# Performance work log

Measured on AMD Instinct MI355X. Metric: run time of the kernel, lower is better.

## Reference

```python
import jax, jax.numpy as jnp
import numpy as np

E = 1024
BUCKET = 16
TAU = 0.75
ITERS = 8
SCALE = E ** -0.5
EPS = 1e-6


def _gumbel(rng, shape):
    u = jax.random.uniform(rng, shape, jnp.float32, 0.0, 1.0)
    return -jnp.log(-jnp.log(u + EPS) + EPS)


def _log_sinkhorn(log_alpha, n_iter):
    def body(i, la):
        la = la - jax.scipy.special.logsumexp(la, axis=-1, keepdims=True)
        la = la - jax.scipy.special.logsumexp(la, axis=-2, keepdims=True)
        return la
    return jnp.exp(jax.lax.fori_loop(0, n_iter, body, log_alpha))


def setup_inputs() -> dict:
    rng = jax.random.key(0)
    ks = jax.random.split(rng, 9)
    T, B, S = 4096, 8, 4096
    w = 0.02
    return {
        "query": jax.random.normal(ks[0], (T, B, E), jnp.float32),
        "key": jax.random.normal(ks[1], (S, B, E), jnp.float32),
        "value": jax.random.normal(ks[2], (S, B, E), jnp.float32),
        "wq": jax.random.normal(ks[3], (E, E), jnp.float32) * w,
        "bq": jnp.zeros((E,), jnp.float32),
        "wk": jax.random.normal(ks[4], (E, E), jnp.float32) * w,
        "bk": jnp.zeros((E,), jnp.float32),
        "wo": jax.random.normal(ks[5], (E, E), jnp.float32) * w,
        "bo": jnp.zeros((E,), jnp.float32),
    }


def reference(query, key, value, wq, bq, wk, bk, wo, bo):
    T, B, _ = query.shape
    S = key.shape[0]
    # projections (Linear: x @ W.T + b), move to (B, T, E)
    q = jnp.einsum('tbe,fe->btf', query, wq) + bq
    k = jnp.einsum('sbe,fe->bsf', key, wk) + bk
    v = jnp.transpose(value, (1, 0, 2))  # (B, S, E)
    nb, nkb = T // BUCKET, S // BUCKET
    # bucket aggregation: mean-pool q/k, flatten v buckets
    qb = q.reshape(B, nb, BUCKET, E).mean(axis=2)          # (B, nb, E)
    kb = k.reshape(B, nkb, BUCKET, E).mean(axis=2)         # (B, nkb, E)
    vb = v.reshape(B, nkb, BUCKET * E)                     # (B, nkb, BUCKET*E)
    # dot energy
    logits = jnp.einsum('bqe,bke->bqk', qb, kb) * SCALE    # (B, nb, nkb)
    log_alpha = logits
    # gumbel-sinkhorn (noise=True)
    g = _gumbel(jax.random.key(42), logits.shape)
    attn_weights = _log_sinkhorn((logits.astype(jnp.float32) + g) / TAU, ITERS)
    # attend on flattened buckets, then un-aggregate
    attn = jnp.einsum('bqk,bkd->bqd', attn_weights, vb)    # (B, nb, BUCKET*E)
    attn = attn.reshape(B, nb * BUCKET, E)
    attn = jnp.transpose(attn, (1, 0, 2))                  # (T, B, E)
    out = jnp.einsum('tbe,fe->tbf', attn, wo) + bo
    return out, attn_weights, log_alpha
```

## Files before the change

kernel.cpp:

```cpp
#include <hip/hip_runtime.h>


typedef float    f32x4 __attribute__((ext_vector_type(4)));
typedef _Float16 h4    __attribute__((ext_vector_type(4)));
typedef _Float16 h8    __attribute__((ext_vector_type(8)));

#define OUT_ELEMS 33554432
#define AW_ELEMS  524288

__device__ __forceinline__ void gload16(const void* g, void* l) {
  __builtin_amdgcn_global_load_lds((__attribute__((address_space(1))) void*)g,
                                   (__attribute__((address_space(3))) void*)l,
                                   16, 0, 0);
}

__global__ __launch_bounds__(256) void cb_k(const float* __restrict__ wq,
                                            const float* __restrict__ wk,
                                            const float* __restrict__ wo,
                                            _Float16* __restrict__ wdst,
                                            const float* __restrict__ q,
                                            const float* __restrict__ k,
                                            _Float16* __restrict__ qbar,
                                            _Float16* __restrict__ kbar) {
  __shared__ __attribute__((aligned(16))) float ldsbuf[8192];
  int bid = blockIdx.x;
  int tid = threadIdx.x;
  if (bid < 3072) {
    int which = bid >> 10;
    const float* src = which == 0 ? wq : (which == 1 ? wk : wo);
    size_t idx = (size_t)(bid & 1023) * 256 + tid;
    f32x4 v = ((const f32x4*)src)[idx];
    ((h4*)(wdst + (size_t)which * 1048576))[idx] = __builtin_convertvector(v, h4);
  } else {
    int g = bid - 3072;
    int srcid = g >> 12, ii = (g >> 4) & 255, bb = (g >> 1) & 7, eh = g & 1;
    const float* s2 = srcid ? k : q;
    _Float16* d2 = srcid ? kbar : qbar;
    const int grp = tid >> 7;
    const int wh  = (tid >> 6) & 1;
    const int col = tid & 127;
    #pragma unroll
    for (int jj = 0; jj < 8; ++jj) {
      int j = jj * 2 + grp;
      gload16(s2 + (size_t)((ii * 16 + j) * 8 + bb) * 1024 + eh * 512 + col * 4,
              &ldsbuf[j * 512 + wh * 256]);
    }
    __syncthreads();
    if (tid < 128) {
      f32x4 a = {0.f, 0.f, 0.f, 0.f};
      #pragma unroll
      for (int j = 0; j < 16; ++j)
        a += *(const f32x4*)&ldsbuf[j * 512 + tid * 4];
      a *= 0.0625f;
      ((h4*)(d2 + (size_t)(bb * 256 + ii) * 1024 + eh * 512))[tid] =
          __builtin_convertvector(a, h4);
    }
  }
}

__device__ __forceinline__ unsigned rotl32(unsigned x, int r) {
  return (x << r) | (x >> (32 - r));
}
__global__ __launch_bounds__(256) void gumbel_k(const float* __restrict__ logits,
                                                float* __restrict__ ebuf) {
  unsigned i = blockIdx.x * 256 + threadIdx.x;
  const unsigned k0 = 0u, k1 = 42u, k2 = 0u ^ 42u ^ 0x1BD11BDAu;
  unsigned x0 = 0u + k0, x1 = i + k1;
#define R4(a,b,c,d) \
  x0 += x1; x1 = rotl32(x1, a); x1 ^= x0; \
  x0 += x1; x1 = rotl32(x1, b); x1 ^= x0; \
  x0 += x1; x1 = rotl32(x1, c); x1 ^= x0; \
  x0 += x1; x1 = rotl32(x1, d); x1 ^= x0;
  R4(13,15,26,6)  x0 += k1; x1 += k2 + 1u;
  R4(17,29,16,24) x0 += k2; x1 += k0 + 2u;
  R4(13,15,26,6)  x0 += k0; x1 += k1 + 3u;
  R4(17,29,16,24) x0 += k1; x1 += k2 + 4u;
  R4(13,15,26,6)  x0 += k2; x1 += k0 + 5u;
#undef R4
  unsigned bits = x0 ^ x1;
  float u = __builtin_bit_cast(float, (bits >> 9) | 0x3f800000u) - 1.0f;
  float g = -logf(-logf(u + 1e-6f) + 1e-6f);
  ebuf[i] = __expf((logits[i] + g) / 0.75f);
}

__global__ __launch_bounds__(1024) void sinkvt_k(const float* __restrict__ ein,
                                                 float* __restrict__ attnw,
                                                 _Float16* __restrict__ wsh,
                                                 const float* __restrict__ v,
                                                 _Float16* __restrict__ vt) {
  __shared__ __attribute__((aligned(16))) char smem[36864];
  const int t = threadIdx.x;
  if (blockIdx.x < 8) {
    const int b = blockIdx.x;
    const int r = t >> 2, p = t & 3;
    const int k = t & 255, g = t >> 8;
    const float* Eb = ein + (size_t)b * 65536;
    const f32x4* Eb4 = (const f32x4*)Eb;
    float* ra = (float*)smem;
    float* cb = ra + 256;
    float (*part)[256] = (float (*)[256])(cb + 256);
    if (t < 256) cb[t] = 1.0f;
    __syncthreads();
    const f32x4* cb4 = (const f32x4*)cb;

    for (int it = 0; it < 8; ++it) {
      float s = 0.f;
      #pragma unroll
      for (int i = 0; i < 16; ++i) {
        f32x4 e = Eb4[r * 64 + p * 16 + i];
        f32x4 c = cb4[p * 16 + i];
        f32x4 m = e * c;
        s += (m[0] + m[1]) + (m[2] + m[3]);
      }
      s += __shfl_xor(s, 1, 64);
      s += __shfl_xor(s, 2, 64);
      if (p == 0) ra[r] = 1.0f / s;
      __syncthreads();
      float s2 = 0.f;
      #pragma unroll 8
      for (int q2 = 0; q2 < 64; ++q2) {
        int row = g * 64 + q2;
        s2 += Eb[row * 256 + k] * ra[row];
      }
      part[g][k] = s2;
      __syncthreads();
      if (t < 256) {
        cb[t] = 1.0f / (part[0][t] + part[1][t] + part[2][t] + part[3][t]);
      }
      __syncthreads();
    }

    const float arow = ra[r];
    f32x4* aw = (f32x4*)(attnw + (size_t)b * 65536 + r * 256 + p * 64);
    h4* wh = (h4*)(wsh + (size_t)b * 65536 + r * 256 + p * 64);
    #pragma unroll
    for (int i = 0; i < 16; ++i) {
      f32x4 e = Eb4[r * 64 + p * 16 + i];
      f32x4 c = cb4[p * 16 + i];
      f32x4 w = e * c * arow;
      aw[i] = w;
      h4 hv;
      hv[0] = (_Float16)w[0]; hv[1] = (_Float16)w[1];
      hv[2] = (_Float16)w[2]; hv[3] = (_Float16)w[3];
      wh[i] = hv;
    }
  } else {
    const int s = t >> 8, t2 = t & 255;
    int bid = (blockIdx.x - 8) * 4 + s;
    _Float16 (*tile)[72] = (_Float16 (*)[72])(smem + s * 9216);
    int kb = bid & 3, eb = (bid >> 2) & 15, j = (bid >> 6) & 15;
    int b = ((bid >> 10) + (bid & 7)) & 7;
    int k0 = kb * 64, e0 = eb * 64;
    int r = t2 >> 2, qq = t2 & 3;
    const float* src = v + ((size_t)((k0 + r) * 16 + j) * 8 + b) * 1024 + e0;
    #pragma unroll
    for (int ii = 0; ii < 4; ++ii) {
      f32x4 x = ((const f32x4*)src)[qq + ii * 4];
      *(h4*)&tile[r][(qq + ii * 4) * 4] = __builtin_convertvector(x, h4);
    }
    __syncthreads();
    _Float16* dstp = vt + (((size_t)(b * 16 + j) * 1024 + e0 + r) * 256 + k0 + qq * 16);
    h8 o0, o1;
    #pragma unroll
    for (int kk = 0; kk < 8; ++kk) o0[kk] = tile[qq * 16 + kk][r];
    #pragma unroll
    for (int kk = 0; kk < 8; ++kk) o1[kk] = tile[qq * 16 + 8 + kk][r];
    *(h8*)dstp = o0;
    *(h8*)(dstp + 8) = o1;
  }
}

template <int MODE>
__global__ __launch_bounds__(256) void gemm128(const _Float16* __restrict__ A,
                                               const _Float16* __restrict__ B,
                                               const float* __restrict__ bias,
                                               const float* __restrict__ bias2,
                                               void* __restrict__ out0,
                                               int K, int lda, int ldb) {
  const int tid = threadIdx.x, lane = tid & 63, w = tid >> 6;
  int bx = blockIdx.x, by = blockIdx.y, bz = blockIdx.z;
  if constexpr (MODE == 0) {
    int wid = ((bx & 7) << 4) + (bx >> 3);
    by = wid & 7; bx = wid >> 3;
  }
  if constexpr (MODE == 2) {
    int wid = ((bx & 7) << 8) + (bx >> 3);
    bz = wid >> 4; by = (wid >> 1) & 7; bx = wid & 1;
  }
  const int m0 = bx * 128, n0 = by * 128;
  const _Float16* Ab = A;
  const _Float16* Bb = B;
  const float* bs = bias;
  if constexpr (MODE == 0) {
    Ab += (size_t)bz * 2097152;
    Bb += (size_t)bz * 1048576;
    if (bz) bs = bias2;
  }
  if constexpr (MODE == 1) { Ab += (size_t)bz * 262144; Bb += (size_t)bz * 262144; }
  if constexpr (MODE == 2) { Ab += (size_t)(bz >> 4) * 65536; Bb += (size_t)bz * 262144; }
  __shared__ _Float16 lA[128 * 32];
  __shared__ _Float16 lB[128 * 32];
  f32x4 acc[4][4] = {};
  const int wm = (w >> 1) * 64, wn = (w & 1) * 64;
  const int fr = lane & 15, fk = (lane >> 4) * 8;
  const int q0 = tid, q1 = tid + 256;

  for (int kt = 0; kt < K; kt += 32) {
    __syncthreads();
    gload16(Ab + (size_t)(m0 + (q0 >> 2)) * lda + kt + (q0 & 3) * 8, &lA[(w * 64) * 8]);
    gload16(Ab + (size_t)(m0 + (q1 >> 2)) * lda + kt + (q1 & 3) * 8, &lA[(256 + w * 64) * 8]);
    gload16(Bb + (size_t)(n0 + (q0 >> 2)) * ldb + kt + (q0 & 3) * 8, &lB[(w * 64) * 8]);
    gload16(Bb + (size_t)(n0 + (q1 >> 2)) * ldb + kt + (q1 & 3) * 8, &lB[(256 + w * 64) * 8]);
    __syncthreads();
    h8 af[4], bf[4];
    #pragma unroll
    for (int i = 0; i < 4; ++i) {
      af[i] = *(const h8*)&lA[(wm + i * 16 + fr) * 32 + fk];
      bf[i] = *(const h8*)&lB[(wn + i * 16 + fr) * 32 + fk];
    }
    #pragma unroll
    for (int mi = 0; mi < 4; ++mi)
      #pragma unroll
      for (int ni = 0; ni < 4; ++ni)
        acc[mi][ni] = __builtin_amdgcn_mfma_f32_16x16x32_f16(af[mi], bf[ni], acc[mi][ni], 0, 0, 0);
  }

  const int er = (lane >> 4) * 4;
  #pragma unroll
  for (int mi = 0; mi < 4; ++mi) {
    #pragma unroll
    for (int ni = 0; ni < 4; ++ni) {
      #pragma unroll
      for (int r = 0; r < 4; ++r) {
        int row = m0 + wm + mi * 16 + er + r;
        int col = n0 + wn + ni * 16 + fr;
        float val = acc[mi][ni][r];
        if constexpr (MODE == 0) {
          ((_Float16*)out0)[(size_t)bz * 2097152 + (size_t)row * 1024 + col] =
              (_Float16)(val + bs[col]);
        } else if constexpr (MODE == 1) {
          ((float*)out0)[(size_t)bz * 65536 + row * 256 + col] = val * 0.03125f;
        } else {
          int b = bz >> 4, j = bz & 15;
          ((_Float16*)out0)[((size_t)(b * 4096 + row * 16 + j)) * 1024 + col] = (_Float16)val;
        }
      }
    }
  }
}

__global__ __launch_bounds__(512, 1) void gemm256_out(const _Float16* __restrict__ A,
                                                      const _Float16* __restrict__ B,
                                                      const float* __restrict__ bias,
                                                      float* __restrict__ out) {
  extern __shared__ __align__(16) _Float16 dsm[];
  _Float16 (*lA)[16384] = (_Float16 (*)[16384])dsm;
  _Float16 (*lB)[16384] = (_Float16 (*)[16384])(dsm + 32768);
  const int tid = threadIdx.x, lane = tid & 63, w = tid >> 6;
  const int wr = w >> 2, wc = w & 3;
  int bx = blockIdx.x;
  int wid = ((bx & 7) << 6) + (bx >> 3);
  const int m0 = (wid >> 2) * 256, n0 = (wid & 3) * 256;
  const int fr = lane & 15, fk = (lane >> 4) * 8;
  const int sx = (lane & 7) << 3;
  const int c0 = fk ^ sx, c1 = (fk + 32) ^ sx;
  f32x4 acc[8][4] = {};

#define STAGE(t, buf) { \
    const int cs = ((tid & 7) ^ ((tid >> 3) & 7)) * 8; \
    const _Float16* Ag = A + (size_t)(m0 + (tid >> 3)) * 1024 + (t) * 64 + cs; \
    const _Float16* Bg = B + (size_t)(n0 + (tid >> 3)) * 1024 + (t) * 64 + cs; \
    _Float16* la0 = &lA[buf][w * 512]; \
    _Float16* lb0 = &lB[buf][w * 512]; \
    gload16(Ag,               la0); \
    gload16(Ag +  64 * 1024,  la0 + 4096); \
    gload16(Ag + 128 * 1024,  la0 + 8192); \
    gload16(Ag + 192 * 1024,  la0 + 12288); \
    gload16(Bg,               lb0); \
    gload16(Bg +  64 * 1024,  lb0 + 4096); \
    gload16(Bg + 128 * 1024,  lb0 + 8192); \
    gload16(Bg + 192 * 1024,  lb0 + 12288); \
  }

  STAGE(0, 0)
  STAGE(1, 1)

  for (int t = 0; t < 16; ++t) {
    const int bt = t & 1;
    if (t < 15) { asm volatile("s_waitcnt vmcnt(8)" ::: "memory"); }
    else        { asm volatile("s_waitcnt vmcnt(0)" ::: "memory"); }
    __builtin_amdgcn_s_barrier();
    h8 a0[8], b0[4];
    #pragma unroll
    for (int mi = 0; mi < 8; ++mi)
      a0[mi] = *(const h8*)&lA[bt][(wr * 128 + mi * 16 + fr) * 64 + c0];
    #pragma unroll
    for (int ni = 0; ni < 4; ++ni)
      b0[ni] = *(const h8*)&lB[bt][(wc * 64 + ni * 16 + fr) * 64 + c0];
    #pragma unroll
    for (int mi = 0; mi < 8; ++mi)
      #pragma unroll
      for (int ni = 0; ni < 4; ++ni)
        acc[mi][ni] = __builtin_amdgcn_mfma_f32_16x16x32_f16(a0[mi], b0[ni], acc[mi][ni], 0, 0, 0);
    h8 a1[8], b1[4];
    #pragma unroll
    for (int mi = 0; mi < 8; ++mi)
      a1[mi] = *(const h8*)&lA[bt][(wr * 128 + mi * 16 + fr) * 64 + c1];
    #pragma unroll
    for (int ni = 0; ni < 4; ++ni)
      b1[ni] = *(const h8*)&lB[bt][(wc * 64 + ni * 16 + fr) * 64 + c1];
    asm volatile("s_waitcnt lgkmcnt(0)" ::: "memory");
    __builtin_amdgcn_sched_barrier(0);
    __builtin_amdgcn_s_barrier();
    if (t + 2 < 16) STAGE(t + 2, bt)
    __builtin_amdgcn_sched_barrier(0);
    __builtin_amdgcn_s_setprio(1);
    #pragma unroll
    for (int mi = 0; mi < 8; ++mi)
      #pragma unroll
      for (int ni = 0; ni < 4; ++ni)
        acc[mi][ni] = __builtin_amdgcn_mfma_f32_16x16x32_f16(a1[mi], b1[ni], acc[mi][ni], 0, 0, 0);
    __builtin_amdgcn_s_setprio(0);
  }
#undef STAGE

  const int er = (lane >> 4) * 4;
  #pragma unroll
  for (int mi = 0; mi < 8; ++mi) {
    #pragma unroll
    for (int ni = 0; ni < 4; ++ni) {
      #pragma unroll
      for (int r = 0; r < 4; ++r) {
        int row = m0 + wr * 128 + mi * 16 + er + r;
        int col = n0 + wc * 64 + ni * 16 + fr;
        int bb = row >> 12, tt = row & 4095;
        out[((size_t)tt * 8 + bb) * 1024 + col] = acc[mi][ni][r] + bias[col];
      }
    }
  }
}

extern "C" void kernel_launch(void* const* d_in, const int* in_sizes, int n_in,
                              void* d_out, int out_size, void* d_ws, size_t ws_size,
                              hipStream_t stream) {
  const float* query = (const float*)d_in[0];
  const float* key   = (const float*)d_in[1];
  const float* value = (const float*)d_in[2];
  const float* wq    = (const float*)d_in[3];
  const float* bq    = (const float*)d_in[4];
  const float* wk    = (const float*)d_in[5];
  const float* bk    = (const float*)d_in[6];
  const float* wo    = (const float*)d_in[7];
  const float* bo    = (const float*)d_in[8];

  float* out      = (float*)d_out;
  float* attnw    = out + OUT_ELEMS;
  float* logalpha = out + OUT_ELEMS + AW_ELEMS;

  char* ws = (char*)d_ws;
  const size_t MB = 1024 * 1024;
  _Float16* wqh   = (_Float16*)(ws + 0 * MB);
  _Float16* woh   = (_Float16*)(ws + 4 * MB);
  _Float16* qbar  = (_Float16*)(ws + 6 * MB);
  _Float16* kbar  = (_Float16*)(ws + 10 * MB);
  _Float16* qbh   = (_Float16*)(ws + 14 * MB);
  _Float16* kbh   = (_Float16*)(ws + 18 * MB);
  float*    ebuf  = (float*)(ws + 22 * MB);
  _Float16* wsh   = (_Float16*)(ws + 25 * MB);
  _Float16* vt    = (_Float16*)(ws + 26 * MB);
  _Float16* attnh = (_Float16*)(ws + 90 * MB);
  (void)in_sizes; (void)n_in; (void)out_size; (void)ws_size;

  cb_k<<<dim3(11264), 256, 0, stream>>>(wq, wk, wo, wqh, query, key, qbar, kbar);

  gemm128<0><<<dim3(128, 1, 2), 256, 0, stream>>>(qbar, wqh, bq, bk, qbh, 1024, 1024, 1024);
  gemm128<1><<<dim3(2, 2, 8), 256, 0, stream>>>(qbh, kbh, nullptr, nullptr, logalpha, 1024, 1024, 1024);

  gumbel_k<<<dim3(2048), 256, 0, stream>>>(logalpha, ebuf);
  sinkvt_k<<<dim3(2056), 1024, 0, stream>>>(ebuf, attnw, wsh, value, vt);

  gemm128<2><<<dim3(2048), 256, 0, stream>>>(wsh, vt, nullptr, nullptr, attnh, 256, 256, 256);
  gemm256_out<<<dim3(512), 512, 131072, stream>>>(attnh, woh, bo, out);
}
```

Before: 323.4 us.

## Fold gumbel noise into sinkhorn kernel and use 256-tile pipelined attention GEMM

Removes the separate gumbel kernel by computing the noise and exp for each batch's logits inside the sinkhorn blocks before iterating. It also replaces the 128x128 attention-times-value GEMM with a 256x256-tile kernel that double-buffers LDS, uses an XOR-swizzled layout and sets wave priority, as the output projection GEMM already does. Together these cut one launch and aim for better MFMA utilisation on the attention GEMM. The trade-off is that the 8 sinkhorn blocks now do the gumbel work serially, and the larger tiles mean fewer blocks in flight.

```diff
diff --git a/kernel.cpp b/kernel.cpp
--- a/kernel.cpp
+++ b/kernel.cpp
@@ -12,6 +12,28 @@
   __builtin_amdgcn_global_load_lds((__attribute__((address_space(1))) void*)g,
                                    (__attribute__((address_space(3))) void*)l,
                                    16, 0, 0);
+}
+
+__device__ __forceinline__ unsigned rotl32(unsigned x, int r) {
+  return (x << r) | (x >> (32 - r));
+}
+__device__ __forceinline__ float gumbel_of(unsigned i) {
+  const unsigned k0 = 0u, k1 = 42u, k2 = 0u ^ 42u ^ 0x1BD11BDAu;
+  unsigned x0 = 0u + k0, x1 = i + k1;
+#define R4(a,b,c,d) \
+  x0 += x1; x1 = rotl32(x1, a); x1 ^= x0; \
+  x0 += x1; x1 = rotl32(x1, b); x1 ^= x0; \
+  x0 += x1; x1 = rotl32(x1, c); x1 ^= x0; \
+  x0 += x1; x1 = rotl32(x1, d); x1 ^= x0;
+  R4(13,15,26,6)  x0 += k1; x1 += k2 + 1u;
+  R4(17,29,16,24) x0 += k2; x1 += k0 + 2u;
+  R4(13,15,26,6)  x0 += k0; x1 += k1 + 3u;
+  R4(17,29,16,24) x0 += k1; x1 += k2 + 4u;
+  R4(13,15,26,6)  x0 += k2; x1 += k0 + 5u;
+#undef R4
+  unsigned bits = x0 ^ x1;
+  float u = __builtin_bit_cast(float, (bits >> 9) | 0x3f800000u) - 1.0f;
+  return -logf(-logf(u + 1e-6f) + 1e-6f);
 }
 
 __global__ __launch_bounds__(256) void cb_k(const float* __restrict__ wq,
@@ -58,32 +80,8 @@
   }
 }
 
-__device__ __forceinline__ unsigned rotl32(unsigned x, int r) {
-  return (x << r) | (x >> (32 - r));
-}
-__global__ __launch_bounds__(256) void gumbel_k(const float* __restrict__ logits,
-                                                float* __restrict__ ebuf) {
-  unsigned i = blockIdx.x * 256 + threadIdx.x;
-  const unsigned k0 = 0u, k1 = 42u, k2 = 0u ^ 42u ^ 0x1BD11BDAu;
-  unsigned x0 = 0u + k0, x1 = i + k1;
-#define R4(a,b,c,d) \
-  x0 += x1; x1 = rotl32(x1, a); x1 ^= x0; \
-  x0 += x1; x1 = rotl32(x1, b); x1 ^= x0; \
-  x0 += x1; x1 = rotl32(x1, c); x1 ^= x0; \
-  x0 += x1; x1 = rotl32(x1, d); x1 ^= x0;
-  R4(13,15,26,6)  x0 += k1; x1 += k2 + 1u;
-  R4(17,29,16,24) x0 += k2; x1 += k0 + 2u;
-  R4(13,15,26,6)  x0 += k0; x1 += k1 + 3u;
-  R4(17,29,16,24) x0 += k1; x1 += k2 + 4u;
-  R4(13,15,26,6)  x0 += k2; x1 += k0 + 5u;
-#undef R4
-  unsigned bits = x0 ^ x1;
-  float u = __builtin_bit_cast(float, (bits >> 9) | 0x3f800000u) - 1.0f;
-  float g = -logf(-logf(u + 1e-6f) + 1e-6f);
-  ebuf[i] = __expf((logits[i] + g) / 0.75f);
-}
-
-__global__ __launch_bounds__(1024) void sinkvt_k(const float* __restrict__ ein,
+__global__ __launch_bounds__(1024) void sinkvt_k(const float* __restrict__ logalpha,
+                                                 float* __restrict__ ebuf,
                                                  float* __restrict__ attnw,
                                                  _Float16* __restrict__ wsh,
                                                  const float* __restrict__ v,
@@ -92,9 +90,15 @@
   const int t = threadIdx.x;
   if (blockIdx.x < 8) {
     const int b = blockIdx.x;
+    for (int u = 0; u < 64; ++u) {
+      unsigned ig = (unsigned)b * 65536 + (unsigned)u * 1024 + t;
+      ebuf[ig] = __expf((logalpha[ig] + gumbel_of(ig)) / 0.75f);
+    }
+    __syncthreads();
+
     const int r = t >> 2, p = t & 3;
     const int k = t & 255, g = t >> 8;
-    const float* Eb = ein + (size_t)b * 65536;
+    const float* Eb = ebuf + (size_t)b * 65536;
     const f32x4* Eb4 = (const f32x4*)Eb;
     float* ra = (float*)smem;
     float* cb = ra + 256;
@@ -183,10 +187,6 @@
     int wid = ((bx & 7) << 4) + (bx >> 3);
     by = wid & 7; bx = wid >> 3;
   }
-  if constexpr (MODE == 2) {
-    int wid = ((bx & 7) << 8) + (bx >> 3);
-    bz = wid >> 4; by = (wid >> 1) & 7; bx = wid & 1;
-  }
   const int m0 = bx * 128, n0 = by * 128;
   const _Float16* Ab = A;
   const _Float16* Bb = B;
@@ -197,7 +197,6 @@
     if (bz) bs = bias2;
   }
   if constexpr (MODE == 1) { Ab += (size_t)bz * 262144; Bb += (size_t)bz * 262144; }
-  if constexpr (MODE == 2) { Ab += (size_t)(bz >> 4) * 65536; Bb += (size_t)bz * 262144; }
   __shared__ _Float16 lA[128 * 32];
   __shared__ _Float16 lB[128 * 32];
   f32x4 acc[4][4] = {};
@@ -238,12 +237,103 @@
         if constexpr (MODE == 0) {
           ((_Float16*)out0)[(size_t)bz * 2097152 + (size_t)row * 1024 + col] =
               (_Float16)(val + bs[col]);
-        } else if constexpr (MODE == 1) {
+        } else {
           ((float*)out0)[(size_t)bz * 65536 + row * 256 + col] = val * 0.03125f;
-        } else {
-          int b = bz >> 4, j = bz & 15;
-          ((_Float16*)out0)[((size_t)(b * 4096 + row * 16 + j)) * 1024 + col] = (_Float16)val;
         }
+      }
+    }
+  }
+}
+
+__global__ __launch_bounds__(512, 1) void gemm256_att(const _Float16* __restrict__ W,
+                                                      const _Float16* __restrict__ V,
+                                                      _Float16* __restrict__ attnh) {
+  extern __shared__ __align__(16) _Float16 dsm[];
+  _Float16 (*lA)[16384] = (_Float16 (*)[16384])dsm;
+  _Float16 (*lB)[16384] = (_Float16 (*)[16384])(dsm + 32768);
+  const int tid = threadIdx.x, lane = tid & 63, w = tid >> 6;
+  const int wr = w >> 2, wc = w & 3;
+  int bx = blockIdx.x;
+  int wid = ((bx & 7) << 6) + (bx >> 3);
+  const int bj = wid >> 2, nt = wid & 3;
+  const int b = bj >> 4, j = bj & 15;
+  const int n0 = nt * 256;
+  const _Float16* A = W + (size_t)b * 65536;
+  const _Float16* B = V + (size_t)bj * 262144;
+  const int fr = lane & 15, fk = (lane >> 4) * 8;
+  const int sx = (lane & 7) << 3;
+  const int c0 = fk ^ sx, c1 = (fk + 32) ^ sx;
+  f32x4 acc[8][4] = {};
+
+#define STAGE(t, buf) { \
+    const int cs = ((tid & 7) ^ ((tid >> 3) & 7)) * 8; \
+    const _Float16* Ag = A + (size_t)(tid >> 3) * 256 + (t) * 64 + cs; \
+    const _Float16* Bg = B + (size_t)(n0 + (tid >> 3)) * 256 + (t) * 64 + cs; \
+    _Float16* la0 = &lA[buf][w * 512]; \
+    _Float16* lb0 = &lB[buf][w * 512]; \
+    gload16(Ag,              la0); \
+    gload16(Ag +  64 * 256,  la0 + 4096); \
+    gload16(Ag + 128 * 256,  la0 + 8192); \
+    gload16(Ag + 192 * 256,  la0 + 12288); \
+    gload16(Bg,              lb0); \
+    gload16(Bg +  64 * 256,  lb0 + 4096); \
+    gload16(Bg + 128 * 256,  lb0 + 8192); \
+    gload16(Bg + 192 * 256,  lb0 + 12288); \
+  }
+
+  STAGE(0, 0)
+  STAGE(1, 1)
+
+  for (int t = 0; t < 4; ++t) {
+    const int bt = t & 1;
+    if (t < 3) { asm volatile("s_waitcnt vmcnt(8)" ::: "memory"); }
+    else       { asm volatile("s_waitcnt vmcnt(0)" ::: "memory"); }
+    __builtin_amdgcn_s_barrier();
+    h8 a0[8], b0[4];
+    #pragma unroll
+    for (int mi = 0; mi < 8; ++mi)
+      a0[mi] = *(const h8*)&lA[bt][(wr * 128 + mi * 16 + fr) * 64 + c0];
+    #pragma unroll
+    for (int ni = 0; ni < 4; ++ni)
+      b0[ni] = *(const h8*)&lB[bt][(wc * 64 + ni * 16 + fr) * 64 + c0];
+    #pragma unroll
+    for (int mi = 0; mi < 8; ++mi)
+      #pragma unroll
+      for (int ni = 0; ni < 4; ++ni)
+        acc[mi][ni] = __builtin_amdgcn_mfma_f32_16x16x32_f16(a0[mi], b0[ni], acc[mi][ni], 0, 0, 0);
+    h8 a1[8], b1[4];
+    #pragma unroll
+    for (int mi = 0; mi < 8; ++mi)
+      a1[mi] = *(const h8*)&lA[bt][(wr * 128 + mi * 16 + fr) * 64 + c1];
+    #pragma unroll
+    for (int ni = 0; ni < 4; ++ni)
+      b1[ni] = *(const h8*)&lB[bt][(wc * 64 + ni * 16 + fr) * 64 + c1];
+    asm volatile("s_waitcnt lgkmcnt(0)" ::: "memory");
+    __builtin_amdgcn_sched_barrier(0);
+    __builtin_amdgcn_s_barrier();
+    if (t + 2 < 4) STAGE(t + 2, bt)
+    __builtin_amdgcn_sched_barrier(0);
+    __builtin_amdgcn_s_setprio(1);
+    #pragma unroll
+    for (int mi = 0; mi < 8; ++mi)
+      #pragma unroll
+      for (int ni = 0; ni < 4; ++ni)
+        acc[mi][ni] = __builtin_amdgcn_mfma_f32_16x16x32_f16(a1[mi], b1[ni], acc[mi][ni], 0, 0, 0);
+    __builtin_amdgcn_s_setprio(0);
+  }
+#undef STAGE
+
+  const int er = (lane >> 4) * 4;
+  #pragma unroll
+  for (int mi = 0; mi < 8; ++mi) {
+    #pragma unroll
+    for (int ni = 0; ni < 4; ++ni) {
+      #pragma unroll
+      for (int r = 0; r < 4; ++r) {
+        int row = wr * 128 + mi * 16 + er + r;
+        int col = n0 + wc * 64 + ni * 16 + fr;
+        attnh[((size_t)(b * 4096 + row * 16 + j)) * 1024 + col] =
+            (_Float16)acc[mi][ni][r];
       }
     }
   }
@@ -376,9 +466,8 @@
   gemm128<0><<<dim3(128, 1, 2), 256, 0, stream>>>(qbar, wqh, bq, bk, qbh, 1024, 1024, 1024);
   gemm128<1><<<dim3(2, 2, 8), 256, 0, stream>>>(qbh, kbh, nullptr, nullptr, logalpha, 1024, 1024, 1024);
 
-  gumbel_k<<<dim3(2048), 256, 0, stream>>>(logalpha, ebuf);
-  sinkvt_k<<<dim3(2056), 1024, 0, stream>>>(ebuf, attnw, wsh, value, vt);
-
-  gemm128<2><<<dim3(2048), 256, 0, stream>>>(wsh, vt, nullptr, nullptr, attnh, 256, 256, 256);
+  sinkvt_k<<<dim3(2056), 1024, 0, stream>>>(logalpha, ebuf, attnw, wsh, value, vt);
+
+  gemm256_att<<<dim3(512), 512, 131072, stream>>>(wsh, vt, attnh);
   gemm256_out<<<dim3(512), 512, 131072, stream>>>(attnh, woh, bo, out);
 }
```

New measurement: 402.5 us. 1.24x slower.
